# Kernel tuning notes

Measured on AMD Instinct MI355X. Metric: run time of the kernel, lower is better.

The kernel has to match this reference:

```python
import jax, jax.numpy as jnp
import numpy as np

PH, PW, K = 32, 32, 2            # block grid and points per block
AROUND, AROUND_R, TOPK = 5, 0.1, 5
NHEAD = 8


def grid_sample(img, grid):
    # img [B,C,H,W]; grid [B,Hg,Wg,2], grid[...,0]=x (width), grid[...,1]=y (height)
    # torch defaults: bilinear, padding_mode='zeros', align_corners=False
    B, C, H, W = img.shape
    gx, gy = grid[..., 0], grid[..., 1]
    ix = ((gx + 1.0) * W - 1.0) * 0.5
    iy = ((gy + 1.0) * H - 1.0) * 0.5
    x0 = jnp.floor(ix)
    y0 = jnp.floor(iy)
    wx1 = ix - x0
    wy1 = iy - y0
    img_f = img.reshape(B, C, H * W)

    def gather(xf, yf):
        valid = (xf >= 0) & (xf <= W - 1) & (yf >= 0) & (yf <= H - 1)
        xi = jnp.clip(xf, 0, W - 1).astype(jnp.int32)
        yi = jnp.clip(yf, 0, H - 1).astype(jnp.int32)
        idx = (yi * W + xi).reshape(B, 1, -1)
        v = jnp.take_along_axis(img_f, jnp.broadcast_to(idx, (B, C, idx.shape[-1])), axis=2)
        v = v.reshape(B, C, *xf.shape[1:])
        return v * valid[:, None].astype(img.dtype)

    out = (gather(x0, y0) * ((1 - wx1) * (1 - wy1))[:, None]
           + gather(x0 + 1, y0) * (wx1 * (1 - wy1))[:, None]
           + gather(x0, y0 + 1) * ((1 - wx1) * wy1)[:, None]
           + gather(x0 + 1, y0 + 1) * (wx1 * wy1)[:, None])
    return out


def blockwise_sample(x, rand):
    # BlockwiseRandomSampler.forward (entirely under torch.no_grad)
    B = x.shape[0]
    bs = 2.0 / PH
    h0 = jnp.linspace(-1.0, 1.0 - bs, PH).reshape(1, PH, 1, 1)
    w0 = jnp.linspace(-1.0, 1.0 - bs, PW).reshape(1, 1, PW, 1)
    c0 = rand[..., 0] * bs + h0          # matches original: dim0 += h_starts
    c1 = rand[..., 1] * bs + w0
    coords = jnp.stack([c0, c1], -1).reshape(B, PH * PW * K, 2)
    pf = grid_sample(x, coords[:, None])[:, :, 0].transpose(0, 2, 1)  # [B,N,C]
    return jax.lax.stop_gradient(coords), jax.lax.stop_gradient(pf)


def soft_align(x1, pf, points, pos2d, arand):
    # pf [B,N,C], points [B,N,2]
    grid = points[:, None] + (arand * 2.0 - 0.5) * 2.0 * AROUND_R   # [B,A,N,2]
    grid = jax.lax.stop_gradient(jnp.clip(grid, -1.0, 1.0))
    emb = grid_sample(pos2d, grid)   # [B,C,A,N]
    af = grid_sample(x1, grid)       # [B,C,A,N]
    rep = jax.lax.stop_gradient(pf.transpose(0, 2, 1)[:, :, None])  # [B,C,1,N]
    num = jnp.sum(rep * af, axis=1)                                  # [B,A,N]
    den = jnp.maximum(jnp.linalg.norm(rep, axis=1), 1e-8) * jnp.maximum(jnp.linalg.norm(af, axis=1), 1e-8)
    w = jax.nn.softmax(num / den, axis=1)[:, None]                   # [B,1,A,N]
    return pf + jnp.sum(emb * w, axis=2).transpose(0, 2, 1)


def layer_norm(x, w, b):
    m = jnp.mean(x, -1, keepdims=True)
    v = jnp.mean((x - m) ** 2, -1, keepdims=True)
    return (x - m) / jnp.sqrt(v + 1e-5) * w + b


def mha(qx, kvx, in_w, in_b, out_w, out_b):
    B, Tq, C = qx.shape
    Tk = kvx.shape[1]
    hd = C // NHEAD
    q = (qx @ in_w[:, :C] + in_b[:C]).reshape(B, Tq, NHEAD, hd)
    k = (kvx @ in_w[:, C:2 * C] + in_b[C:2 * C]).reshape(B, Tk, NHEAD, hd)
    v = (kvx @ in_w[:, 2 * C:] + in_b[2 * C:]).reshape(B, Tk, NHEAD, hd)
    att = jax.nn.softmax(jnp.einsum('bqhd,bkhd->bhqk', q, k) * (1.0 / hd ** 0.5), axis=-1)
    o = jnp.einsum('bhqk,bkhd->bqhd', att, v).reshape(B, Tq, C)
    return o @ out_w + out_b


def _forward(mainx, others, position_embedding, modality_query, s_w1, s_b1, s_w2, s_b2,
             sa_in_w, sa_in_b, sa_out_w, sa_out_b, ca_in_w, ca_in_b, ca_out_w, ca_out_b,
             ff1_w, ff1_b, ff2_w, ff2_b, ln_w, ln_b, block_rand, around_rand):
    B, C, H, W = mainx.shape
    pos2d = jnp.broadcast_to(position_embedding.reshape(1, H, W, C).transpose(0, 3, 1, 2), (B, C, H, W))
    feats = []
    for i, x in enumerate(others):
        coords, pf = blockwise_sample(x, block_rand[i])
        score = jax.nn.sigmoid(jax.nn.relu(pf @ s_w1 + s_b1) @ s_w2 + s_b2)[..., 0]  # [B,N]
        idx = jax.lax.top_k(score, TOPK)[1]                                           # no_grad topk
        px = jnp.take_along_axis(coords, jnp.broadcast_to(idx[..., None], (B, TOPK, 2)), axis=1)
        pfk = jnp.take_along_axis(pf, jnp.broadcast_to(idx[..., None], (B, TOPK, C)), axis=1)
        apf = soft_align(mainx, pfk, px, pos2d, around_rand[i])
        feats.append(apf + modality_query[:, i + 1:i + 2])
    mem = jnp.concatenate(feats, axis=1)  # [B, M*TOPK, C]
    tgt = mainx.transpose(0, 2, 3, 1).reshape(B, H * W, C) + modality_query[:, 0:1] + position_embedding
    for l in range(sa_in_w.shape[0]):  # post-norm nn.TransformerDecoderLayer, relu, eval mode
        tgt = layer_norm(tgt + mha(tgt, tgt, sa_in_w[l], sa_in_b[l], sa_out_w[l], sa_out_b[l]), ln_w[l, 0], ln_b[l, 0])
        tgt = layer_norm(tgt + mha(tgt, mem, ca_in_w[l], ca_in_b[l], ca_out_w[l], ca_out_b[l]), ln_w[l, 1], ln_b[l, 1])
        tgt = layer_norm(tgt + (jax.nn.relu(tgt @ ff1_w[l] + ff1_b[l]) @ ff2_w[l] + ff2_b[l]), ln_w[l, 2], ln_b[l, 2])
    return tgt.reshape(B, H, W, C).transpose(0, 3, 1, 2)  # score_loss path is 0 (no gt/ps segments)


def setup_inputs():
    key = jax.random.key(0)
    ks = jax.random.split(key, 16)
    B, C, H, W, L, FF, M = 8, 768, 32, 32, 2, 3072, 2
    n = jax.random.normal
    d = {
        'mainx': n(ks[0], (B, C, H, W), jnp.float32),
        'other0': n(ks[1], (B, C, H, W), jnp.float32),
        'other1': n(ks[2], (B, C, H, W), jnp.float32),
        'position_embedding': 0.02 * n(ks[3], (1, H * W, C), jnp.float32),
        'modality_query': (0.02 * n(ks[4], (1, M + 1, C), jnp.float32)).at[:, 0].set(0.0),  # padding_idx=0
        's_w1': 0.02 * n(ks[5], (C, C), jnp.float32),
        's_b1': jnp.zeros((C,), jnp.float32),
        's_w2': 0.02 * n(ks[6], (C, 1), jnp.float32),
        's_b2': jnp.zeros((1,), jnp.float32),
        'sa_in_w': 0.02 * n(ks[7], (L, C, 3 * C), jnp.float32),
        'sa_in_b': jnp.zeros((L, 3 * C), jnp.float32),
        'sa_out_w': 0.02 * n(ks[8], (L, C, C), jnp.float32),
        'sa_out_b': jnp.zeros((L, C), jnp.float32),
        'ca_in_w': 0.02 * n(ks[9], (L, C, 3 * C), jnp.float32),
        'ca_in_b': jnp.zeros((L, 3 * C), jnp.float32),
        'ca_out_w': 0.02 * n(ks[10], (L, C, C), jnp.float32),
        'ca_out_b': jnp.zeros((L, C), jnp.float32),
        'ff1_w': 0.02 * n(ks[11], (L, C, FF), jnp.float32),
        'ff1_b': jnp.zeros((L, FF), jnp.float32),
        'ff2_w': 0.02 * n(ks[12], (L, FF, C), jnp.float32),
        'ff2_b': jnp.zeros((L, C), jnp.float32),
        'ln_w': jnp.ones((L, 3, C), jnp.float32),
        'ln_b': jnp.zeros((L, 3, C), jnp.float32),
        'block_rand': jax.random.uniform(ks[13], (M, B, PH, PW, K, 2), jnp.float32),
        'around_rand': jax.random.uniform(ks[14], (M, B, AROUND, TOPK, 2), jnp.float32),
    }
    return d


def reference(mainx, other0, other1, position_embedding, modality_query, s_w1, s_b1, s_w2, s_b2,
              sa_in_w, sa_in_b, sa_out_w, sa_out_b, ca_in_w, ca_in_b, ca_out_w, ca_out_b,
              ff1_w, ff1_b, ff2_w, ff2_b, ln_w, ln_b, block_rand, around_rand):
    return _forward(mainx, (other0, other1), position_embedding, modality_query, s_w1, s_b1, s_w2, s_b2,
                    sa_in_w, sa_in_b, sa_out_w, sa_out_b, ca_in_w, ca_in_b, ca_out_w, ca_out_b,
                    ff1_w, ff1_b, ff2_w, ff2_b, ln_w, ln_b, block_rand, around_rand)
```

## Files before the change

kernel.cpp:

```cpp
#include <hip/hip_runtime.h>
#include <hip/hip_bf16.h>
#include <math.h>

typedef __hip_bfloat16 hbf16;

#define B_ 8
#define C_ 768
#define HW_ 1024
#define NH_ 8
#define HD_ 96
#define NPTS 2048
#define AROUND_ 5
#define TOPK_ 5
#define MOD_ 2
#define FF_ 3072
#define TOK_ (B_*HW_)

typedef __attribute__((ext_vector_type(8))) short short8v;
typedef __attribute__((ext_vector_type(4))) short short4v;
typedef __attribute__((ext_vector_type(4))) float f32x4;

__device__ __forceinline__ float b2f(hbf16 v){ return __bfloat162float(v); }

__device__ __forceinline__ void gload16(const void* g, void* l) {
  __builtin_amdgcn_global_load_lds(
      (const __attribute__((address_space(1))) void*)g,
      (__attribute__((address_space(3))) void*)l, 16, 0, 0);
}

struct Taps { int x0,x1,y0,y1; float w00,w10,w01,w11; };
__device__ __forceinline__ Taps bilin_taps(float gx, float gy) {
  Taps t;
  float ix = ((gx+1.f)*32.f - 1.f)*0.5f;
  float iy = ((gy+1.f)*32.f - 1.f)*0.5f;
  float x0f = floorf(ix), y0f = floorf(iy);
  float wx1 = ix-x0f, wy1 = iy-y0f, wx0 = 1.f-wx1, wy0 = 1.f-wy1;
  int x0=(int)x0f, y0=(int)y0f, x1=x0+1, y1=y0+1;
  bool vx0=(x0>=0)&&(x0<=31), vx1=(x1>=0)&&(x1<=31);
  bool vy0=(y0>=0)&&(y0<=31), vy1=(y1>=0)&&(y1<=31);
  t.w00 = (vx0&&vy0) ? wx0*wy0 : 0.f;
  t.w10 = (vx1&&vy0) ? wx1*wy0 : 0.f;
  t.w01 = (vx0&&vy1) ? wx0*wy1 : 0.f;
  t.w11 = (vx1&&vy1) ? wx1*wy1 : 0.f;
  t.x0 = min(max(x0,0),31); t.x1 = min(max(x1,0),31);
  t.y0 = min(max(y0,0),31); t.y1 = min(max(y1,0),31);
  return t;
}

__device__ __forceinline__ float block_reduce_sum_256(float v, float* red) {
  int tid = threadIdx.x;
  red[tid] = v; __syncthreads();
  for (int s = 128; s > 0; s >>= 1) { if (tid < s) red[tid] += red[tid+s]; __syncthreads(); }
  float r = red[0]; __syncthreads();
  return r;
}

__global__ __launch_bounds__(256) void f2b_kernel(const float* __restrict__ in,
    hbf16* __restrict__ out, int n) {
  int i = (blockIdx.x*256 + threadIdx.x)*4;
  if (i >= n) return;
  float4 v = *(const float4*)&in[i];
  out[i+0] = __float2bfloat16(v.x);
  out[i+1] = __float2bfloat16(v.y);
  out[i+2] = __float2bfloat16(v.z);
  out[i+3] = __float2bfloat16(v.w);
}

__global__ __launch_bounds__(256) void wtrans_kernel(const float* __restrict__ in,
    hbf16* __restrict__ out, int K, int N) {
  __shared__ float t[32][33];
  int tx = threadIdx.x & 31, ty = threadIdx.x >> 5;
  int k0 = blockIdx.y*32, n0 = blockIdx.x*32;
  #pragma unroll
  for (int i = 0; i < 32; i += 8) t[ty+i][tx] = in[(size_t)(k0+ty+i)*N + n0+tx];
  __syncthreads();
  #pragma unroll
  for (int i = 0; i < 32; i += 8)
    out[(size_t)(n0+ty+i)*K + k0 + tx] = __float2bfloat16(t[tx][ty+i]);
}

__global__ __launch_bounds__(256) void wtrans_split_kernel(const float* __restrict__ in,
    hbf16* __restrict__ hi, hbf16* __restrict__ lo, int K, int N) {
  __shared__ float t[32][33];
  int tx = threadIdx.x & 31, ty = threadIdx.x >> 5;
  int k0 = blockIdx.y*32, n0 = blockIdx.x*32;
  #pragma unroll
  for (int i = 0; i < 32; i += 8) t[ty+i][tx] = in[(size_t)(k0+ty+i)*N + n0+tx];
  __syncthreads();
  #pragma unroll
  for (int i = 0; i < 32; i += 8) {
    float v = t[tx][ty+i];
    hbf16 h = __float2bfloat16(v);
    hi[(size_t)(n0+ty+i)*K + k0 + tx] = h;
    lo[(size_t)(n0+ty+i)*K + k0 + tx] = __float2bfloat16(v - b2f(h));
  }
}

__global__ __launch_bounds__(256) void btrans_kernel(const float* __restrict__ in,
    float* __restrict__ out, int R, int S) {
  __shared__ float t[32][33];
  int tx = threadIdx.x & 31, ty = threadIdx.x >> 5;
  int r0 = blockIdx.y*32, s0 = blockIdx.x*32;
  const float* ib = in + (size_t)blockIdx.z*R*S;
  float* ob = out + (size_t)blockIdx.z*R*S;
  #pragma unroll
  for (int i = 0; i < 32; i += 8) t[ty+i][tx] = ib[(size_t)(r0+ty+i)*S + s0+tx];
  __syncthreads();
  #pragma unroll
  for (int i = 0; i < 32; i += 8) ob[(size_t)(s0+ty+i)*R + r0+tx] = t[tx][ty+i];
}

__global__ __launch_bounds__(256) void zero_kernel(float* __restrict__ p, int n) {
  int i = blockIdx.x*256 + threadIdx.x;
  if (i < n) p[i] = 0.f;
}

__global__ __launch_bounds__(256) void sample_all_kernel(const float* __restrict__ oT,
    const float* __restrict__ brand, hbf16* __restrict__ pf_hi, hbf16* __restrict__ pf_lo,
    float* __restrict__ coords_all, int g0) {
  int ly = blockIdx.x;
  int inst = g0 + ly;
  int b = inst & 7;
  const float* xT = oT + (size_t)b*HW_*C_;
  int tid = threadIdx.x;
  int p = tid >> 6, lane = tid & 63;
  int n = blockIdx.y*4 + p;
  int k = n & 1, pw = (n >> 1) & 31, ph = n >> 6;
  const float* br = brand + (size_t)inst*4096;
  int roff = ((ph*32 + pw)*2 + k)*2;
  float r0 = br[roff], r1 = br[roff+1];
  const float bs = 0.0625f;
  float c0 = r0*bs + ((float)ph*bs - 1.0f);
  float c1 = r1*bs + ((float)pw*bs - 1.0f);
  Taps t = bilin_taps(c0, c1);
  const float* r00 = xT + (size_t)(t.y0*32+t.x0)*C_;
  const float* r10 = xT + (size_t)(t.y0*32+t.x1)*C_;
  const float* r01 = xT + (size_t)(t.y1*32+t.x0)*C_;
  const float* r11 = xT + (size_t)(t.y1*32+t.x1)*C_;
  size_t base = ((size_t)ly*NPTS + n)*C_;
  short* ph_ = (short*)pf_hi;
  short* pl_ = (short*)pf_lo;
  #pragma unroll
  for (int kk = 0; kk < 3; ++kk) {
    int c = kk*256 + lane*4;
    float4 v00 = *(const float4*)(r00 + c);
    float4 v10 = *(const float4*)(r10 + c);
    float4 v01 = *(const float4*)(r01 + c);
    float4 v11 = *(const float4*)(r11 + c);
    float o[4];
    o[0] = t.w00*v00.x + t.w10*v10.x + t.w01*v01.x + t.w11*v11.x;
    o[1] = t.w00*v00.y + t.w10*v10.y + t.w01*v01.y + t.w11*v11.y;
    o[2] = t.w00*v00.z + t.w10*v10.z + t.w01*v01.z + t.w11*v11.z;
    o[3] = t.w00*v00.w + t.w10*v10.w + t.w01*v01.w + t.w11*v11.w;
    short4v hs, ls;
    #pragma unroll
    for (int e = 0; e < 4; ++e) {
      hbf16 h = __float2bfloat16(o[e]);
      hs[e] = *(short*)&h;
      hbf16 l = __float2bfloat16(o[e] - b2f(h));
      ls[e] = *(short*)&l;
    }
    *(short4v*)&ph_[base + c] = hs;
    *(short4v*)&pl_[base + c] = ls;
  }
  if (lane == 0) {
    size_t co = ((size_t)inst*NPTS + n)*2;
    coords_all[co] = c0; coords_all[co+1] = c1;
  }
}

__device__ __forceinline__ void xcd_tile(int gx, int gy, int& row, int& col) {
  int wgid = blockIdx.y * gx + blockIdx.x;
  int xcd = wgid & 7;
  int li = wgid >> 3;
  row = xcd * (gy >> 3) + li / gx;
  col = li % gx;
}

__global__ __launch_bounds__(256) void score_gemm_kernel(const short* __restrict__ Ahi,
    const short* __restrict__ Alo, const short* __restrict__ Bhi, const short* __restrict__ Blo,
    const float* __restrict__ b1, const float* __restrict__ w2, float* __restrict__ logit) {
  __shared__ short AsH[128*32];
  __shared__ short AsL[128*32];
  __shared__ short BsH[128*32];
  __shared__ short BsL[128*32];
  int tid = threadIdx.x;
  int lane = tid & 63, w = tid >> 6;
  int wr = (w >> 1) * 64, wc = (w & 1) * 64;
  int m16 = lane & 15, quad = lane >> 4, q8 = quad * 8;
  int brow, bcol;
  xcd_tile(gridDim.x, gridDim.y, brow, bcol);
  int bm = brow * 128, bn = bcol * 128;
  int sr = w * 32;
  int lr = lane >> 2, lc = (lane & 3) * 8;
  f32x4 acc[4][4] = {};
  for (int k0 = 0; k0 < 768; k0 += 32) {
    {
      const short* pa = &Ahi[(size_t)(bm + sr + lr)*768 + k0 + lc];
      const short* pl = &Alo[(size_t)(bm + sr + lr)*768 + k0 + lc];
      const short* pb = &Bhi[(size_t)(bn + sr + lr)*768 + k0 + lc];
      const short* pq = &Blo[(size_t)(bn + sr + lr)*768 + k0 + lc];
      gload16(pa,            &AsH[sr*32]);
      gload16(pa + 16*768,   &AsH[(sr+16)*32]);
      gload16(pl,            &AsL[sr*32]);
      gload16(pl + 16*768,   &AsL[(sr+16)*32]);
      gload16(pb,            &BsH[sr*32]);
      gload16(pb + 16*768,   &BsH[(sr+16)*32]);
      gload16(pq,            &BsL[sr*32]);
      gload16(pq + 16*768,   &BsL[(sr+16)*32]);
    }
    __syncthreads();
    short8v ah[4], al[4], bh[4], bl[4];
    #pragma unroll
    for (int i=0;i<4;++i) {
      ah[i] = *(const short8v*)&AsH[(wr + i*16 + m16)*32 + q8];
      al[i] = *(const short8v*)&AsL[(wr + i*16 + m16)*32 + q8];
      bh[i] = *(const short8v*)&BsH[(wc + i*16 + m16)*32 + q8];
      bl[i] = *(const short8v*)&BsL[(wc + i*16 + m16)*32 + q8];
    }
    #pragma unroll
    for (int i=0;i<4;++i)
      #pragma unroll
      for (int j=0;j<4;++j) {
        acc[i][j] = __builtin_amdgcn_mfma_f32_16x16x32_bf16(ah[i], bh[j], acc[i][j], 0, 0, 0);
        acc[i][j] = __builtin_amdgcn_mfma_f32_16x16x32_bf16(ah[i], bl[j], acc[i][j], 0, 0, 0);
        acc[i][j] = __builtin_amdgcn_mfma_f32_16x16x32_bf16(al[i], bh[j], acc[i][j], 0, 0, 0);
      }
    __syncthreads();
  }
  float b1v[4], w2v[4];
  #pragma unroll
  for (int j=0;j<4;++j) {
    int col = bn + wc + j*16 + m16;
    b1v[j] = b1[col]; w2v[j] = w2[col];
  }
  #pragma unroll
  for (int i=0;i<4;++i) {
    #pragma unroll
    for (int r=0;r<4;++r) {
      float v = 0.f;
      #pragma unroll
      for (int j=0;j<4;++j) {
        float h = fmaxf(acc[i][j][r] + b1v[j], 0.f);
        v += h * w2v[j];
      }
      v += __shfl_xor(v, 1); v += __shfl_xor(v, 2);
      v += __shfl_xor(v, 4); v += __shfl_xor(v, 8);
      if (m16 == 0) atomicAdd(&logit[bm + wr + i*16 + quad*4 + r], v);
    }
  }
}

__global__ void topk_all_kernel(const float* __restrict__ logit, int* __restrict__ idx) {
  int lane = threadIdx.x;
  const float* score = logit + (size_t)blockIdx.x*NPTS;
  float v[32];
  #pragma unroll
  for (int i = 0; i < 32; ++i) v[i] = score[(i<<6) | lane];
  for (int t = 0; t < TOPK_; ++t) {
    float bv = v[0]; int bi = lane;
    #pragma unroll
    for (int i = 1; i < 32; ++i) { if (v[i] > bv) { bv = v[i]; bi = (i<<6)|lane; } }
    for (int off = 32; off; off >>= 1) {
      float ov = __shfl_xor(bv, off);
      int   oi = __shfl_xor(bi, off);
      if (ov > bv || (ov == bv && oi < bi)) { bv = ov; bi = oi; }
    }
    if (lane == 0) idx[blockIdx.x*8 + t] = bi;
    if ((bi & 63) == lane) v[bi >> 6] = -1e30f;
  }
}

__global__ __launch_bounds__(256) void softalign_all_kernel(const float* __restrict__ mainxT,
    const float* __restrict__ pos, const hbf16* __restrict__ pf_hi, const hbf16* __restrict__ pf_lo,
    const float* __restrict__ coords_all, const int* __restrict__ idx_all,
    const float* __restrict__ arand, const float* __restrict__ mq,
    float* __restrict__ memf, int g0) {
  int t = blockIdx.x;
  int ly = blockIdx.y;
  int inst = g0 + ly;
  int mod = inst >> 3, b = inst & 7;
  const float* mT_b = mainxT + (size_t)b*HW_*C_;
  const float* arand_ib = arand + (size_t)inst*AROUND_*TOPK_*2;
  const float* coords = coords_all + (size_t)inst*NPTS*2;
  int tid = threadIdx.x;
  int n = idx_all[ly*8 + t];
  float px0 = coords[n*2], px1 = coords[n*2+1];
  size_t pfb = ((size_t)ly*NPTS + n)*C_;
  float pfv[3];
  #pragma unroll
  for (int i=0;i<3;++i) {
    int c = tid + i*256;
    pfv[i] = b2f(pf_hi[pfb + c]) + b2f(pf_lo[pfb + c]);
  }
  __shared__ float red[256];
  float pp = block_reduce_sum_256(pfv[0]*pfv[0]+pfv[1]*pfv[1]+pfv[2]*pfv[2], red);
  float embr[AROUND_][3];
  float num_a[AROUND_], aa_a[AROUND_];
  for (int a=0; a<AROUND_; ++a) {
    int ar = (a*TOPK_ + t)*2;
    float g0c = px0 + (arand_ib[ar]*2.f - 0.5f)*0.2f;
    float g1c = px1 + (arand_ib[ar+1]*2.f - 0.5f)*0.2f;
    g0c = fminf(fmaxf(g0c,-1.f),1.f);
    g1c = fminf(fmaxf(g1c,-1.f),1.f);
    Taps tp = bilin_taps(g0c, g1c);
    int i00=tp.y0*32+tp.x0, i10=tp.y0*32+tp.x1, i01=tp.y1*32+tp.x0, i11=tp.y1*32+tp.x1;
    float s_num = 0.f, s_aa = 0.f;
    #pragma unroll
    for (int i=0;i<3;++i) {
      int c = tid + i*256;
      float af = tp.w00*mT_b[(size_t)i00*C_+c] + tp.w10*mT_b[(size_t)i10*C_+c]
               + tp.w01*mT_b[(size_t)i01*C_+c] + tp.w11*mT_b[(size_t)i11*C_+c];
      float em = tp.w00*pos[(size_t)i00*C_+c] + tp.w10*pos[(size_t)i10*C_+c]
               + tp.w01*pos[(size_t)i01*C_+c] + tp.w11*pos[(size_t)i11*C_+c];
      embr[a][i] = em;
      s_num += pfv[i]*af;
      s_aa  += af*af;
    }
    num_a[a] = block_reduce_sum_256(s_num, red);
    aa_a[a]  = block_reduce_sum_256(s_aa, red);
  }
  float pn = fmaxf(sqrtf(pp), 1e-8f);
  float w[AROUND_]; float mx = -1e30f;
  #pragma unroll
  for (int a=0;a<AROUND_;++a){ float den = pn * fmaxf(sqrtf(aa_a[a]),1e-8f); w[a]=num_a[a]/den; mx=fmaxf(mx,w[a]); }
  float se = 0.f;
  #pragma unroll
  for (int a=0;a<AROUND_;++a){ w[a]=expf(w[a]-mx); se+=w[a]; }
  float inv = 1.f/se;
  float* mo = memf + ((size_t)b*(MOD_*TOPK_) + mod*TOPK_ + t)*C_;
  #pragma unroll
  for (int i=0;i<3;++i) {
    int c = tid + i*256;
    float o = pfv[i];
    #pragma unroll
    for (int a=0;a<AROUND_;++a) o += embr[a][i]*(w[a]*inv);
    o += mq[(size_t)(mod+1)*C_ + c];
    mo[c] = o;
  }
}

#define BM 64
#define BN 64
#define BK 16
__global__ __launch_bounds__(256) void gemm_kernel(const float* __restrict__ A, int lda,
    const float* __restrict__ Bw, int ldb, const float* __restrict__ bias,
    float* __restrict__ Cm, int ldc, int M, int N, int K, int act) {
  __shared__ float As[BK][BM];
  __shared__ float Bs[BK][BN];
  int tid = threadIdx.x;
  int bm = blockIdx.y * BM, bn = blockIdx.x * BN;
  int arw = tid >> 2, acl = (tid & 3) << 2;
  int brw = tid >> 4, bcl = (tid & 15) << 2;
  int ty = tid >> 4, tx = tid & 15;
  float acc[4][4] = {{0.f}};
  for (int k0 = 0; k0 < K; k0 += BK) {
    float a0=0.f,a1=0.f,a2=0.f,a3=0.f;
    if (bm + arw < M) {
      const float* ap = A + (size_t)(bm+arw)*lda + k0 + acl;
      a0=ap[0]; a1=ap[1]; a2=ap[2]; a3=ap[3];
    }
    As[acl+0][arw]=a0; As[acl+1][arw]=a1; As[acl+2][arw]=a2; As[acl+3][arw]=a3;
    const float* bp = Bw + (size_t)(k0+brw)*ldb + bn + bcl;
    Bs[brw][bcl+0]=bp[0]; Bs[brw][bcl+1]=bp[1]; Bs[brw][bcl+2]=bp[2]; Bs[brw][bcl+3]=bp[3];
    __syncthreads();
    #pragma unroll
    for (int kk = 0; kk < BK; ++kk) {
      float4 av = *reinterpret_cast<const float4*>(&As[kk][ty<<2]);
      float4 bv = *reinterpret_cast<const float4*>(&Bs[kk][tx<<2]);
      acc[0][0]+=av.x*bv.x; acc[0][1]+=av.x*bv.y; acc[0][2]+=av.x*bv.z; acc[0][3]+=av.x*bv.w;
      acc[1][0]+=av.y*bv.x; acc[1][1]+=av.y*bv.y; acc[1][2]+=av.y*bv.z; acc[1][3]+=av.y*bv.w;
      acc[2][0]+=av.z*bv.x; acc[2][1]+=av.z*bv.y; acc[2][2]+=av.z*bv.z; acc[2][3]+=av.z*bv.w;
      acc[3][0]+=av.w*bv.x; acc[3][1]+=av.w*bv.y; acc[3][2]+=av.w*bv.z; acc[3][3]+=av.w*bv.w;
    }
    __syncthreads();
  }
  #pragma unroll
  for (int i=0;i<4;++i) {
    int r = bm + (ty<<2) + i;
    if (r >= M) continue;
    float* cp = Cm + (size_t)r*ldc + bn + (tx<<2);
    #pragma unroll
    for (int j=0;j<4;++j) {
      float v = acc[i][j] + bias[bn + (tx<<2) + j];
      if (act) v = fmaxf(v, 0.f);
      cp[j] = v;
    }
  }
}

__global__ __launch_bounds__(256) void gemm_mfma_t(const short* __restrict__ A, int lda,
    const short* __restrict__ Bt, int ldbt, const float* __restrict__ bias,
    hbf16* __restrict__ Cm, int ldc, int K, int act) {
  __shared__ short As[128*32];
  __shared__ short Bs[128*32];
  int tid = threadIdx.x;
  int lane = tid & 63, w = tid >> 6;
  int wr = (w >> 1) * 64, wc = (w & 1) * 64;
  int m16 = lane & 15, q8 = (lane >> 4) * 8;
  int brow, bcol;
  xcd_tile(gridDim.x, gridDim.y, brow, bcol);
  int bm = brow * 128, bn = bcol * 128;
  int sr = w * 32;
  int lr = lane >> 2, lc = (lane & 3) * 8;
  f32x4 acc[4][4] = {};
  for (int k0 = 0; k0 < K; k0 += 32) {
    {
      const short* pa = &A [(size_t)(bm + sr + lr)*lda  + k0 + lc];
      const short* pb = &Bt[(size_t)(bn + sr + lr)*ldbt + k0 + lc];
      gload16(pa,                    &As[sr*32]);
      gload16(pa + (size_t)16*lda,   &As[(sr+16)*32]);
      gload16(pb,                    &Bs[sr*32]);
      gload16(pb + (size_t)16*ldbt,  &Bs[(sr+16)*32]);
    }
    __syncthreads();
    short8v af[4], bf[4];
    #pragma unroll
    for (int i=0;i<4;++i) af[i] = *(const short8v*)&As[(wr + i*16 + m16)*32 + q8];
    #pragma unroll
    for (int j=0;j<4;++j) bf[j] = *(const short8v*)&Bs[(wc + j*16 + m16)*32 + q8];
    #pragma unroll
    for (int i=0;i<4;++i)
      #pragma unroll
      for (int j=0;j<4;++j)
        acc[i][j] = __builtin_amdgcn_mfma_f32_16x16x32_bf16(af[i], bf[j], acc[i][j], 0, 0, 0);
    __syncthreads();
  }
  #pragma unroll
  for (int j=0;j<4;++j) {
    int col = bn + wc + j*16 + m16;
    float bs = bias[col];
    #pragma unroll
    for (int i=0;i<4;++i) {
      int row0 = bm + wr + i*16 + (lane>>4)*4;
      #pragma unroll
      for (int r=0;r<4;++r) {
        float v = acc[i][j][r] + bs;
        if (act) v = fmaxf(v, 0.f);
        Cm[(size_t)(row0+r)*ldc + col] = __float2bfloat16(v);
      }
    }
  }
}

__global__ __launch_bounds__(256) void gemm_mfma_t64(const short* __restrict__ A, int lda,
    const short* __restrict__ Bt, int ldbt, const float* __restrict__ bias,
    hbf16* __restrict__ Cm, int ldc, int K, int act) {
  __shared__ short As[128*32];
  __shared__ short Bs[64*32];
  int tid = threadIdx.x;
  int lane = tid & 63, w = tid >> 6;
  int m16 = lane & 15, q8 = (lane >> 4) * 8;
  int brow, bcol;
  xcd_tile(gridDim.x, gridDim.y, brow, bcol);
  int bm = brow * 128, bn = bcol * 64;
  int sr = w * 32;
  int srB = w * 16;
  int lr = lane >> 2, lc = (lane & 3) * 8;
  f32x4 acc[2][4] = {};
  for (int k0 = 0; k0 < K; k0 += 32) {
    {
      const short* pa = &A [(size_t)(bm + sr  + lr)*lda  + k0 + lc];
      const short* pb = &Bt[(size_t)(bn + srB + lr)*ldbt + k0 + lc];
      gload16(pa,                   &As[sr*32]);
      gload16(pa + (size_t)16*lda,  &As[(sr+16)*32]);
      gload16(pb,                   &Bs[srB*32]);
    }
    __syncthreads();
    short8v af[2], bf[4];
    #pragma unroll
    for (int i=0;i<2;++i) af[i] = *(const short8v*)&As[(w*32 + i*16 + m16)*32 + q8];
    #pragma unroll
    for (int j=0;j<4;++j) bf[j] = *(const short8v*)&Bs[(j*16 + m16)*32 + q8];
    #pragma unroll
    for (int i=0;i<2;++i)
      #pragma unroll
      for (int j=0;j<4;++j)
        acc[i][j] = __builtin_amdgcn_mfma_f32_16x16x32_bf16(af[i], bf[j], acc[i][j], 0, 0, 0);
    __syncthreads();
  }
  #pragma unroll
  for (int j=0;j<4;++j) {
    int col = bn + j*16 + m16;
    float bs = bias[col];
    #pragma unroll
    for (int i=0;i<2;++i) {
      int row0 = bm + w*32 + i*16 + (lane>>4)*4;
      #pragma unroll
      for (int r=0;r<4;++r) {
        float v = acc[i][j][r] + bs;
        if (act) v = fmaxf(v, 0.f);
        Cm[(size_t)(row0+r)*ldc + col] = __float2bfloat16(v);
      }
    }
  }
}

__global__ __launch_bounds__(512, 4) void flash_attn_kernel(const hbf16* __restrict__ qkv_all,
    hbf16* __restrict__ o_all) {
  const int hb = blockIdx.x;
  const int h  = hb & 7;
  const int bz = hb >> 3;
  const int q0 = blockIdx.y * 128;
  const short* qkv = (const short*)(qkv_all + (size_t)bz*HW_*2304);
  hbf16* ob = o_all + (size_t)bz*HW_*C_;
  const int tid = threadIdx.x;
  const int lane = tid & 63, w = tid >> 6;
  const int m16 = lane & 15, quad = lane >> 4, q8 = quad * 8;
  const float scale = 0.10206207261596577f;

  __shared__ short lds[16128];
  short* KP = lds;
  short* Vt = lds + 9216;

  for (int idx = tid; idx < 128*12; idx += 512) {
    int row = idx / 12, dc = idx % 12;
    *(short8v*)&lds[row*104 + dc*8] = *(const short8v*)&qkv[(size_t)(q0+row)*2304 + h*HD_ + dc*8];
  }
  __syncthreads();
  short8v qf[3];
  #pragma unroll
  for (int kkk=0;kkk<3;++kkk)
    qf[kkk] = *(const short8v*)&lds[(w*16 + m16)*104 + q8 + kkk*32];
  __syncthreads();

  float m_st[4], l_st[4];
  f32x4 o_acc[6] = {};
  #pragma unroll
  for (int r=0;r<4;++r){ m_st[r] = -1e30f; l_st[r] = 0.f; }

  for (int t = 0; t < 16; ++t) {
    int j0 = t * 64;
    for (int idx = tid; idx < 64*12; idx += 512) {
      int row = idx / 12, dc = idx % 12;
      *(short8v*)&KP[row*104 + dc*8] = *(const short8v*)&qkv[(size_t)(j0+row)*2304 + C_ + h*HD_ + dc*8];
    }
    for (int idx = tid; idx < 64*12; idx += 512) {
      int j = idx & 63, dc = idx >> 6;
      short8v v = *(const short8v*)&qkv[(size_t)(j0+j)*2304 + 2*C_ + h*HD_ + dc*8];
      #pragma unroll
      for (int s = 0; s < 8; ++s) Vt[(dc*8+s)*72 + j] = v[s];
    }
    __syncthreads();

    f32x4 accs[4] = {};
    #pragma unroll
    for (int kkk = 0; kkk < 3; ++kkk) {
      int kk = kkk*32;
      short8v bf[4];
      #pragma unroll
      for (int n=0;n<4;++n) bf[n] = *(const short8v*)&KP[(n*16 + m16)*104 + q8 + kk];
      #pragma unroll
      for (int n=0;n<4;++n)
        accs[n] = __builtin_amdgcn_mfma_f32_16x16x32_bf16(qf[kkk], bf[n], accs[n], 0, 0, 0);
    }
    __syncthreads();

    #pragma unroll
    for (int r=0;r<4;++r) {
      float mx = -1e30f;
      #pragma unroll
      for (int n=0;n<4;++n) mx = fmaxf(mx, accs[n][r]*scale);
      #pragma unroll
      for (int off=1; off<16; off<<=1) mx = fmaxf(mx, __shfl_xor(mx, off));
      float m_new = fmaxf(m_st[r], mx);
      float alpha = __expf(m_st[r] - m_new);
      float psum = 0.f;
      int prow = (w*16 + quad*4 + r)*72 + m16;
      #pragma unroll
      for (int n=0;n<4;++n) {
        float pv = __expf(accs[n][r]*scale - m_new);
        psum += pv;
        *(hbf16*)&KP[prow + n*16] = __float2bfloat16(pv);
      }
      #pragma unroll
      for (int off=1; off<16; off<<=1) psum += __shfl_xor(psum, off);
      l_st[r] = l_st[r]*alpha + psum;
      m_st[r] = m_new;
      #pragma unroll
      for (int dt=0; dt<6; ++dt) o_acc[dt][r] *= alpha;
    }

    #pragma unroll
    for (int k0 = 0; k0 < 64; k0 += 32) {
      short8v pf_, vf[6];
      pf_ = *(const short8v*)&KP[(w*16 + m16)*72 + q8 + k0];
      #pragma unroll
      for (int dt=0; dt<6; ++dt) vf[dt] = *(const short8v*)&Vt[(dt*16 + m16)*72 + q8 + k0];
      #pragma unroll
      for (int dt=0; dt<6; ++dt)
        o_acc[dt] = __builtin_amdgcn_mfma_f32_16x16x32_bf16(pf_, vf[dt], o_acc[dt], 0, 0, 0);
    }
    __syncthreads();
  }

  #pragma unroll
  for (int r=0;r<4;++r) {
    float inv = 1.f / l_st[r];
    int row = q0 + w*16 + quad*4 + r;
    #pragma unroll
    for (int dt=0; dt<6; ++dt)
      ob[(size_t)row*C_ + h*HD_ + dt*16 + m16] = __float2bfloat16(o_acc[dt][r]*inv);
  }
}

__global__ __launch_bounds__(128) void cross_attn_kernel(hbf16* __restrict__ qb,
    const float* __restrict__ kvm, int b0) {
  int row = blockIdx.x;
  int lb = blockIdx.y;
  int b = b0 + lb;
  int tid = threadIdx.x;
  __shared__ float sc[16];
  __shared__ float qs[C_];
  hbf16* qp = qb + ((size_t)lb*HW_ + row)*C_;
  for (int c = tid; c < C_; c += 128) qs[c] = b2f(qp[c]);
  __syncthreads();
  const float scale = 0.10206207261596577f;
  for (int h = 0; h < NH_; ++h) {
    if (tid < 10) {
      const float* kp = kvm + (size_t)(b*10 + tid)*1536 + h*HD_;
      float s = 0.f;
      for (int d = 0; d < HD_; ++d) s += qs[h*HD_+d]*kp[d];
      sc[tid] = s*scale;
    }
    __syncthreads();
    if (tid == 0) {
      float m = -1e30f;
      for (int j=0;j<10;++j) m = fmaxf(m, sc[j]);
      float se = 0.f;
      for (int j=0;j<10;++j){ sc[j]=expf(sc[j]-m); se+=sc[j]; }
      float inv = 1.f/se;
      for (int j=0;j<10;++j) sc[j]*=inv;
    }
    __syncthreads();
    if (tid < HD_) {
      const float* vp = kvm + (size_t)(b*10)*1536 + C_ + h*HD_ + tid;
      float acc = 0.f;
      for (int j=0;j<10;++j) acc += sc[j]*vp[(size_t)j*1536];
      qp[h*HD_+tid] = __float2bfloat16(acc);
    }
    __syncthreads();
  }
}

__global__ __launch_bounds__(256) void tgt0_kernel(float* __restrict__ tgt,
    const float* __restrict__ mq, const float* __restrict__ pos) {
  size_t i = ((size_t)blockIdx.x*256 + threadIdx.x)*4;
  if (i >= (size_t)TOK_*C_) return;
  int c = (int)(i % C_);
  int tpos = (int)((i / C_) % HW_);
  float4 v = *(float4*)&tgt[i];
  float4 m = *(const float4*)&mq[c];
  float4 pp = *(const float4*)&pos[(size_t)tpos*C_ + c];
  v.x += m.x + pp.x; v.y += m.y + pp.y;
  v.z += m.z + pp.z; v.w += m.w + pp.w;
  *(float4*)&tgt[i] = v;
}

__global__ __launch_bounds__(256) void ln_res_kernel(float* __restrict__ tgt, const hbf16* __restrict__ add,
    const float* __restrict__ w, const float* __restrict__ bvec) {
  __shared__ float red[256];
  int row = blockIdx.x, tid = threadIdx.x;
  float* tp = tgt + (size_t)row*C_;
  const hbf16* ap = add + (size_t)row*C_;
  float x[3]; float s = 0.f, s2 = 0.f;
  #pragma unroll
  for (int i=0;i<3;++i){ int c=tid+i*256; float v=tp[c]+b2f(ap[c]); x[i]=v; s+=v; s2+=v*v; }
  s  = block_reduce_sum_256(s,  red);
  s2 = block_reduce_sum_256(s2, red);
  float mean = s * (1.f/C_);
  float var  = s2 * (1.f/C_) - mean*mean;
  float rstd = rsqrtf(var + 1e-5f);
  #pragma unroll
  for (int i=0;i<3;++i){ int c=tid+i*256; tp[c] = (x[i]-mean)*rstd*w[c] + bvec[c]; }
}

extern "C" void kernel_launch(void* const* d_in, const int* in_sizes, int n_in,
                              void* d_out, int out_size, void* d_ws, size_t ws_size,
                              hipStream_t stream) {
  const float* mainx   = (const float*)d_in[0];
  const float* other0  = (const float*)d_in[1];
  const float* other1  = (const float*)d_in[2];
  const float* pos     = (const float*)d_in[3];
  const float* mq      = (const float*)d_in[4];
  const float* s_w1    = (const float*)d_in[5];
  const float* s_b1    = (const float*)d_in[6];
  const float* s_w2    = (const float*)d_in[7];
  const float* sa_in_w = (const float*)d_in[9];
  const float* sa_in_b = (const float*)d_in[10];
  const float* sa_out_w= (const float*)d_in[11];
  const float* sa_out_b= (const float*)d_in[12];
  const float* ca_in_w = (const float*)d_in[13];
  const float* ca_in_b = (const float*)d_in[14];
  const float* ca_out_w= (const float*)d_in[15];
  const float* ca_out_b= (const float*)d_in[16];
  const float* ff1_w   = (const float*)d_in[17];
  const float* ff1_b   = (const float*)d_in[18];
  const float* ff2_w   = (const float*)d_in[19];
  const float* ff2_b   = (const float*)d_in[20];
  const float* ln_w    = (const float*)d_in[21];
  const float* ln_b    = (const float*)d_in[22];
  const float* brand   = (const float*)d_in[23];
  const float* arand   = (const float*)d_in[24];

  char* p = (char*)d_ws;
  auto alloc = [&](size_t bytes) { char* r = p; p += (bytes + 255) & ~(size_t)255; return (void*)r; };
  float* tgt    = (float*)alloc((size_t)TOK_*C_*4);
  hbf16* wb0    = (hbf16*)alloc((size_t)2359296*2);
  hbf16* wb1    = (hbf16*)alloc((size_t)2359296*2);
  hbf16* w1t_hi = (hbf16*)alloc((size_t)C_*C_*2);
  hbf16* w1t_lo = (hbf16*)alloc((size_t)C_*C_*2);
  float* kvm    = (float*)alloc((size_t)80*1536*4);
  float* memf   = (float*)alloc((size_t)80*C_*4);
  float* coords = (float*)alloc((size_t)16*NPTS*2*4);
  float* logit  = (float*)alloc((size_t)16*NPTS*4);
  int*   idxb   = (int*)alloc(16*8*4);
  char*  S      = p;
  size_t used = (size_t)(p - (char*)d_ws);
  size_t Savail = (ws_size > used) ? ws_size - used : 0;
  int CH = 1;
  if (Savail >= (size_t)8*1024*9216 + 4096) CH = 8;
  else if (Savail >= (size_t)4*1024*9216 + 4096) CH = 4;
  else if (Savail >= (size_t)2*1024*9216 + 4096) CH = 2;
  const size_t R = (size_t)CH*1024;
  const size_t perG = (size_t)NPTS*C_*2*2;
  const size_t oTb = (size_t)B_*HW_*C_*4;
  float* oT = (float*)S;
  char* Spf = S + oTb;
  size_t SA = (Savail > oTb) ? Savail - oTb : 0;
  int G = 1;
  if (SA >= 8*perG) G = 8;
  else if (SA >= 4*perG) G = 4;
  else if (SA >= 2*perG) G = 2;

  btrans_kernel<<<dim3(HW_/32, C_/32, B_), 256, 0, stream>>>(mainx, tgt, C_, HW_);
  wtrans_split_kernel<<<dim3(C_/32, C_/32), 256, 0, stream>>>(s_w1, w1t_hi, w1t_lo, C_, C_);
  zero_kernel<<<16*NPTS/256, 256, 0, stream>>>(logit, 16*NPTS);
  for (int g0 = 0; g0 < 16; g0 += G) {
    if ((g0 & 7) == 0)
      btrans_kernel<<<dim3(HW_/32, C_/32, B_), 256, 0, stream>>>(g0 < 8 ? other0 : other1,
          oT, C_, HW_);
    hbf16* pf_hi = (hbf16*)Spf;
    hbf16* pf_lo = pf_hi + (size_t)G*NPTS*C_;
    sample_all_kernel<<<dim3(G, NPTS/4), 256, 0, stream>>>(oT, brand,
        pf_hi, pf_lo, coords, g0);
    score_gemm_kernel<<<dim3(6, G*16), 256, 0, stream>>>((const short*)pf_hi, (const short*)pf_lo,
        (const short*)w1t_hi, (const short*)w1t_lo, s_b1, s_w2, logit + (size_t)g0*NPTS);
    topk_all_kernel<<<G, 64, 0, stream>>>(logit + (size_t)g0*NPTS, idxb + g0*8);
    softalign_all_kernel<<<dim3(TOPK_, G), 256, 0, stream>>>(tgt, pos, pf_hi, pf_lo,
        coords, idxb + g0*8, arand, mq, memf, g0);
  }

  size_t total = (size_t)TOK_*C_;
  tgt0_kernel<<<(int)((total/4+255)/256), 256, 0, stream>>>(tgt, mq, pos);

  for (int l = 0; l < 2; ++l) {
    wtrans_kernel<<<dim3(3*C_/32, C_/32), 256, 0, stream>>>(sa_in_w + (size_t)l*C_*3*C_, wb0, C_, 3*C_);
    wtrans_kernel<<<dim3(C_/32, C_/32), 256, 0, stream>>>(sa_out_w + (size_t)l*C_*C_, wb1, C_, C_);
    for (int c0 = 0; c0 < B_; c0 += CH) {
      float* tgtc = tgt + (size_t)c0*HW_*C_;
      hbf16* abuf = (hbf16*)S;
      hbf16* qkv  = abuf + R*C_;
      hbf16* oatt = qkv + R*3*C_;
      hbf16* tmpb = oatt + R*C_;
      f2b_kernel<<<(int)((R*C_/4+255)/256), 256, 0, stream>>>(tgtc, abuf, (int)(R*C_));
      gemm_mfma_t<<<dim3(3*C_/128, (int)(R/128)), 256, 0, stream>>>((const short*)abuf, C_,
          (const short*)wb0, C_, sa_in_b + (size_t)l*3*C_, qkv, 3*C_, C_, 0);
      flash_attn_kernel<<<dim3(NH_*CH, HW_/128), 512, 0, stream>>>(qkv, oatt);
      gemm_mfma_t64<<<dim3(C_/64, (int)(R/128)), 256, 0, stream>>>((const short*)oatt, C_,
          (const short*)wb1, C_, sa_out_b + (size_t)l*C_, tmpb, C_, C_, 0);
      ln_res_kernel<<<(int)R, 256, 0, stream>>>(tgtc, tmpb,
          ln_w + (size_t)(l*3+0)*C_, ln_b + (size_t)(l*3+0)*C_);
    }

    wtrans_kernel<<<dim3(C_/32, C_/32), 256, 0, stream>>>(ca_in_w + (size_t)l*C_*3*C_, wb0, C_, 3*C_);
    wtrans_kernel<<<dim3(C_/32, C_/32), 256, 0, stream>>>(ca_out_w + (size_t)l*C_*C_, wb1, C_, C_);
    gemm_kernel<<<dim3((2*C_+BN-1)/BN, (80+BM-1)/BM), 256, 0, stream>>>(memf, C_,
        ca_in_w + (size_t)l*C_*3*C_ + C_, 3*C_, ca_in_b + (size_t)l*3*C_ + C_, kvm, 2*C_,
        80, 2*C_, C_, 0);
    for (int c0 = 0; c0 < B_; c0 += CH) {
      float* tgtc = tgt + (size_t)c0*HW_*C_;
      hbf16* abuf = (hbf16*)S;
      hbf16* qb   = abuf + R*C_;
      hbf16* tmpb = qb + R*C_;
      f2b_kernel<<<(int)((R*C_/4+255)/256), 256, 0, stream>>>(tgtc, abuf, (int)(R*C_));
      gemm_mfma_t64<<<dim3(C_/64, (int)(R/128)), 256, 0, stream>>>((const short*)abuf, C_,
          (const short*)wb0, C_, ca_in_b + (size_t)l*3*C_, qb, C_, C_, 0);
      cross_attn_kernel<<<dim3(HW_, CH), 128, 0, stream>>>(qb, kvm, c0);
      gemm_mfma_t64<<<dim3(C_/64, (int)(R/128)), 256, 0, stream>>>((const short*)qb, C_,
          (const short*)wb1, C_, ca_out_b + (size_t)l*C_, tmpb, C_, C_, 0);
      ln_res_kernel<<<(int)R, 256, 0, stream>>>(tgtc, tmpb,
          ln_w + (size_t)(l*3+1)*C_, ln_b + (size_t)(l*3+1)*C_);
    }

    wtrans_kernel<<<dim3(FF_/32, C_/32), 256, 0, stream>>>(ff1_w + (size_t)l*C_*FF_, wb0, C_, FF_);
    wtrans_kernel<<<dim3(C_/32, FF_/32), 256, 0, stream>>>(ff2_w + (size_t)l*FF_*C_, wb1, FF_, C_);
    for (int c0 = 0; c0 < B_; c0 += CH) {
      float* tgtc = tgt + (size_t)c0*HW_*C_;
      hbf16* abuf = (hbf16*)S;
      hbf16* ffh  = abuf + R*C_;
      hbf16* tmpb = ffh + R*FF_;
      f2b_kernel<<<(int)((R*C_/4+255)/256), 256, 0, stream>>>(tgtc, abuf, (int)(R*C_));
      gemm_mfma_t<<<dim3(FF_/128, (int)(R/128)), 256, 0, stream>>>((const short*)abuf, C_,
          (const short*)wb0, C_, ff1_b + (size_t)l*FF_, ffh, FF_, C_, 1);
      gemm_mfma_t64<<<dim3(C_/64, (int)(R/128)), 256, 0, stream>>>((const short*)ffh, FF_,
          (const short*)wb1, FF_, ff2_b + (size_t)l*C_, tmpb, C_, FF_, 0);
      ln_res_kernel<<<(int)R, 256, 0, stream>>>(tgtc, tmpb,
          ln_w + (size_t)(l*3+2)*C_, ln_b + (size_t)(l*3+2)*C_);
    }
  }

  btrans_kernel<<<dim3(C_/32, HW_/32, B_), 256, 0, stream>>>(tgt, (float*)d_out, HW_, C_);
}
```

Before: 1.483 ms.

## Rewrite cross-attention as one wavefront per query row with shuffle reductions

The cross-attention kernel changes from one 128-thread block per query row, with serial per-head loops, single-thread softmax and many __syncthreads, to one 64-lane wavefront per row. Each lane owns 12 channels, and groups of 8 lanes cover one 96-wide head. Scores are reduced with xor shuffles, the softmax is computed redundantly in registers, and K/V are read with float4 loads. This removes shared memory traffic, barriers and the idle threads of the old version, at the cost of more registers per lane and using __expf instead of expf.

```diff
diff --git a/kernel.cpp b/kernel.cpp
--- a/kernel.cpp
+++ b/kernel.cpp
@@ -604,42 +604,63 @@
   }
 }
 
-__global__ __launch_bounds__(128) void cross_attn_kernel(hbf16* __restrict__ qb,
+__global__ __launch_bounds__(256) void cross_attn_kernel(hbf16* __restrict__ qb,
     const float* __restrict__ kvm, int b0) {
-  int row = blockIdx.x;
+  int wv = threadIdx.x >> 6, lane = threadIdx.x & 63;
+  int row = blockIdx.x*4 + wv;
   int lb = blockIdx.y;
   int b = b0 + lb;
-  int tid = threadIdx.x;
-  __shared__ float sc[16];
-  __shared__ float qs[C_];
+  const float scale = 0.10206207261596577f;
   hbf16* qp = qb + ((size_t)lb*HW_ + row)*C_;
-  for (int c = tid; c < C_; c += 128) qs[c] = b2f(qp[c]);
-  __syncthreads();
-  const float scale = 0.10206207261596577f;
-  for (int h = 0; h < NH_; ++h) {
-    if (tid < 10) {
-      const float* kp = kvm + (size_t)(b*10 + tid)*1536 + h*HD_;
-      float s = 0.f;
-      for (int d = 0; d < HD_; ++d) s += qs[h*HD_+d]*kp[d];
-      sc[tid] = s*scale;
-    }
-    __syncthreads();
-    if (tid == 0) {
-      float m = -1e30f;
-      for (int j=0;j<10;++j) m = fmaxf(m, sc[j]);
-      float se = 0.f;
-      for (int j=0;j<10;++j){ sc[j]=expf(sc[j]-m); se+=sc[j]; }
-      float inv = 1.f/se;
-      for (int j=0;j<10;++j) sc[j]*=inv;
-    }
-    __syncthreads();
-    if (tid < HD_) {
-      const float* vp = kvm + (size_t)(b*10)*1536 + C_ + h*HD_ + tid;
-      float acc = 0.f;
-      for (int j=0;j<10;++j) acc += sc[j]*vp[(size_t)j*1536];
-      qp[h*HD_+tid] = __float2bfloat16(acc);
-    }
-    __syncthreads();
+  int c0 = lane*12;
+  const short* qs = (const short*)qp;
+  float q[12];
+  #pragma unroll
+  for (int i0 = 0; i0 < 3; ++i0) {
+    short4v s = *(const short4v*)&qs[c0 + i0*4];
+    #pragma unroll
+    for (int e = 0; e < 4; ++e) { hbf16 hh; *(short*)&hh = s[e]; q[i0*4+e] = b2f(hh); }
+  }
+  const float* kb = kvm + (size_t)(b*10)*1536;
+  float sc[10];
+  #pragma unroll
+  for (int j = 0; j < 10; ++j) {
+    const float* kp = kb + (size_t)j*1536 + c0;
+    float4 k0 = *(const float4*)(kp);
+    float4 k1 = *(const float4*)(kp+4);
+    float4 k2 = *(const float4*)(kp+8);
+    float s = q[0]*k0.x + q[1]*k0.y + q[2]*k0.z + q[3]*k0.w
+            + q[4]*k1.x + q[5]*k1.y + q[6]*k1.z + q[7]*k1.w
+            + q[8]*k2.x + q[9]*k2.y + q[10]*k2.z + q[11]*k2.w;
+    s += __shfl_xor(s, 1); s += __shfl_xor(s, 2); s += __shfl_xor(s, 4);
+    sc[j] = s * scale;
+  }
+  float m = sc[0];
+  #pragma unroll
+  for (int j=1;j<10;++j) m = fmaxf(m, sc[j]);
+  float se = 0.f;
+  #pragma unroll
+  for (int j=0;j<10;++j){ sc[j] = __expf(sc[j]-m); se += sc[j]; }
+  float inv = 1.f/se;
+  float o[12] = {};
+  #pragma unroll
+  for (int j = 0; j < 10; ++j) {
+    const float* vp = kb + (size_t)j*1536 + C_ + c0;
+    float4 v0 = *(const float4*)(vp);
+    float4 v1 = *(const float4*)(vp+4);
+    float4 v2 = *(const float4*)(vp+8);
+    float pj = sc[j]*inv;
+    o[0]+=pj*v0.x; o[1]+=pj*v0.y; o[2]+=pj*v0.z; o[3]+=pj*v0.w;
+    o[4]+=pj*v1.x; o[5]+=pj*v1.y; o[6]+=pj*v1.z; o[7]+=pj*v1.w;
+    o[8]+=pj*v2.x; o[9]+=pj*v2.y; o[10]+=pj*v2.z; o[11]+=pj*v2.w;
+  }
+  short* qw = (short*)qp;
+  #pragma unroll
+  for (int i0 = 0; i0 < 3; ++i0) {
+    short4v ov;
+    #pragma unroll
+    for (int e = 0; e < 4; ++e) { hbf16 hh = __float2bfloat16(o[i0*4+e]); ov[e] = *(short*)&hh; }
+    *(short4v*)&qw[c0 + i0*4] = ov;
   }
 }
 
@@ -786,7 +807,7 @@
       f2b_kernel<<<(int)((R*C_/4+255)/256), 256, 0, stream>>>(tgtc, abuf, (int)(R*C_));
       gemm_mfma_t64<<<dim3(C_/64, (int)(R/128)), 256, 0, stream>>>((const short*)abuf, C_,
           (const short*)wb0, C_, ca_in_b + (size_t)l*3*C_, qb, C_, C_, 0);
-      cross_attn_kernel<<<dim3(HW_, CH), 128, 0, stream>>>(qb, kvm, c0);
+      cross_attn_kernel<<<dim3(HW_/4, CH), 256, 0, stream>>>(qb, kvm, c0);
       gemm_mfma_t64<<<dim3(C_/64, (int)(R/128)), 256, 0, stream>>>((const short*)qb, C_,
           (const short*)wb1, C_, ca_out_b + (size_t)l*C_, tmpb, C_, C_, 0);
       ln_res_kernel<<<(int)R, 256, 0, stream>>>(tgtc, tmpb,
```

New measurement: 1.388 ms. 1.07x faster.
